# Kernel optimization log

Hardware: AMD Instinct MI355X
Metric: run time of the kernel (lower is better)

The kernel has to match this reference:

```python
import jax, jax.numpy as jnp
import numpy as np

B, M, H2, OUT = 32, 256, 32, 8  # H2 = 2*hidden_features

def setup_inputs() -> dict:
    key = jax.random.key(0)
    k1, k2, k3, k4, k5, k6 = jax.random.split(key, 6)
    x = jax.random.normal(k1, (B, M, 3), dtype=jnp.float32)
    mask = jax.random.randint(k2, (B, M, 1), 0, 2, dtype=jnp.int32)
    W1 = jax.random.normal(k3, (H2, 3), dtype=jnp.float32) * 0.1
    b1 = jax.random.normal(k4, (H2,), dtype=jnp.float32) * 0.1
    W2 = jax.random.normal(k5, (OUT, H2), dtype=jnp.float32) * 0.1
    b2 = jax.random.normal(k6, (OUT,), dtype=jnp.float32) * 0.1
    return {"x": x, "mask": mask, "W1": W1, "b1": b1, "W2": W2, "b2": b2}

def _safe_log(v):
    return jnp.log(jnp.where(v > 0, v, 1.0))

def reference(x, mask, W1, b1, W2, b2):
    # x: [B,M,3] = (eta, phi, log_pt); mask: [B,M,1]
    m = mask.astype(jnp.float32)
    me = (m @ jnp.swapaxes(m, -1, -2))[..., None]          # [B,M,M,1]

    eta, phi, ept = x[..., 0], x[..., 1], jnp.exp(x[..., 2])
    d_eta = eta[:, :, None] - eta[:, None, :]               # [B,M,M]
    d_phi = phi[:, :, None] - phi[:, None, :]
    dr2 = d_eta * d_eta + d_phi * d_phi

    # log dR (get_dr, is_log=True)
    dr_log = (0.5 * _safe_log(dr2))[..., None] * me
    # log kT (get_kt, is_log=True): min(pt_i, pt_j) * dR(linear, masked)
    dr_lin = jnp.sqrt(dr2)[..., None] * me
    kt = jnp.minimum(ept[:, :, None], ept[:, None, :])[..., None] * dr_lin
    kt_log = _safe_log(kt) * me
    # log m^2 (get_mass, is_log=True)
    m2 = 2.0 * ept[:, :, None] * ept[:, None, :] * (jnp.cosh(d_eta) - jnp.cos(d_phi))
    mass_log = _safe_log(m2)[..., None] * me

    feat = jnp.concatenate([mass_log, dr_log, kt_log], axis=-1)  # [B,M,M,3]

    h = jax.nn.leaky_relu(feat @ W1.T + b1, negative_slope=0.01)  # [B,M,M,H2]
    o = (h @ W2.T + b2) * me                                      # [B,M,M,OUT]
    # rearrange 'b n1 n2 h -> (b h) n1 n2'
    return jnp.transpose(o, (0, 3, 1, 2)).reshape(B * OUT, M, M)
```

## Files before the change

kernel.cpp:

```cpp
#include <hip/hip_runtime.h>
#include <math.h>

#define BB 32
#define MM 256
#define H2 32
#define NOUT 8

__device__ __forceinline__ float sinh_mag(float t) {
    float a  = fabsf(t);
    float e  = __expf(a);
    float big = 0.5f * (e - __builtin_amdgcn_rcpf(e));
    float t2 = t * t;
    float small = t + t * t2 * (1.0f/6.0f + t2 * (1.0f/120.0f));
    return (a < 0.5f) ? small : big;
}

__device__ __forceinline__ float sin_mag(float t) {
    float a  = fabsf(t);
    float t2 = t * t;
    float small = t + t * t2 * (-1.0f/6.0f + t2 * (1.0f/120.0f));
    float big = __sinf(t);
    return (a < 0.5f) ? small : big;
}

__global__ __launch_bounds__(256) void interaction_kernel(
    const float* __restrict__ x, const int* __restrict__ mask,
    const float* __restrict__ W1, const float* __restrict__ b1,
    const float* __restrict__ W2, const float* __restrict__ b2,
    float* __restrict__ out)
{
    const int bid = blockIdx.x;
    const int nb  = (bid & 7) * 1024 + (bid >> 3);
    const int b   = nb >> 8;
    const int i   = nb & 255;
    const int j   = threadIdx.x;

    float* op = out + ((size_t)(b * NOUT)) * (MM * MM) + (size_t)i * MM + j;
    const int PSTRIDE = MM * MM;

    const int mi = mask[b * MM + i];
    if (mi == 0) {
        #pragma unroll
        for (int p = 0; p < NOUT; ++p)
            __builtin_nontemporal_store(0.f, op + p * PSTRIDE);
        return;
    }

    const float eta_i = x[(b * MM + i) * 3 + 0];
    const float phi_i = x[(b * MM + i) * 3 + 1];
    const float lpt_i = x[(b * MM + i) * 3 + 2];

    const float eta_j = x[(b * MM + j) * 3 + 0];
    const float phi_j = x[(b * MM + j) * 3 + 1];
    const float lpt_j = x[(b * MM + j) * 3 + 2];
    const float mf    = mask[b * MM + j] ? 1.f : 0.f;

    const float dx  = eta_i - eta_j;
    const float dy  = phi_i - phi_j;
    const float dr2 = dx * dx + dy * dy;

    const float L      = (dr2 > 0.f) ? 0.5f * __logf(dr2) : 0.f;
    const float fdr    = L;
    const float fkt    = (dr2 > 0.f) ? fminf(lpt_i, lpt_j) + L : 0.f;

    const float sh = sinh_mag(0.5f * dx);
    const float sn = sin_mag(0.5f * dy);
    const float c  = 2.0f * (sh * sh + sn * sn);
    const float fmass = (c > 0.f) ? __logf(2.0f * c) + lpt_i + lpt_j : 0.f;

    float o[NOUT];
    #pragma unroll
    for (int p = 0; p < NOUT; ++p) o[p] = b2[p];

    #pragma unroll
    for (int k = 0; k < H2; ++k) {
        float z = b1[k];
        z = fmaf(fmass, W1[k * 3 + 0], z);
        z = fmaf(fdr,   W1[k * 3 + 1], z);
        z = fmaf(fkt,   W1[k * 3 + 2], z);
        z = (z >= 0.f) ? z : 0.01f * z;
        #pragma unroll
        for (int p = 0; p < NOUT; ++p)
            o[p] = fmaf(z, W2[p * H2 + k], o[p]);
    }

    #pragma unroll
    for (int p = 0; p < NOUT; ++p)
        __builtin_nontemporal_store(o[p] * mf, op + p * PSTRIDE);
}

extern "C" void kernel_launch(void* const* d_in, const int* in_sizes, int n_in,
                              void* d_out, int out_size, void* d_ws, size_t ws_size,
                              hipStream_t stream) {
    const float* x    = (const float*)d_in[0];
    const int*   mask = (const int*)d_in[1];
    const float* W1   = (const float*)d_in[2];
    const float* b1   = (const float*)d_in[3];
    const float* W2   = (const float*)d_in[4];
    const float* b2   = (const float*)d_in[5];
    float* out = (float*)d_out;

    dim3 grid(BB * MM);
    dim3 block(MM);
    interaction_kernel<<<grid, block, 0, stream>>>(x, mask, W1, b1, W2, b2, out);
}
```

Measured before the change: 24.53 us.

## Process four rows per block and stage outputs in LDS for float4 stores

Each block now handles four i-rows with 1024 threads. Results go into a shared-memory tile and are written back as float4 vectors covering 4 contiguous rows per output plane. This aims to cut the number of blocks and widen the global stores. In exchange it adds a __syncthreads and 32KB of LDS per block, and drops the nontemporal store hint and the early exit for masked rows.

New measurement: 55.37 us. +125.7%, slower.

```diff
diff --git a/kernel.cpp b/kernel.cpp
--- a/kernel.cpp
+++ b/kernel.cpp
@@ -23,70 +23,82 @@
     return (a < 0.5f) ? small : big;
 }
 
-__global__ __launch_bounds__(256) void interaction_kernel(
+__global__ __launch_bounds__(1024, 8) void interaction_kernel(
     const float* __restrict__ x, const int* __restrict__ mask,
     const float* __restrict__ W1, const float* __restrict__ b1,
     const float* __restrict__ W2, const float* __restrict__ b2,
     float* __restrict__ out)
 {
+    __shared__ float tile[NOUT * 4 * MM];
+
     const int bid = blockIdx.x;
-    const int nb  = (bid & 7) * 1024 + (bid >> 3);
-    const int b   = nb >> 8;
-    const int i   = nb & 255;
-    const int j   = threadIdx.x;
+    const int nb  = (bid & 7) * 256 + (bid >> 3);
+    const int b   = nb >> 6;
+    const int i0  = (nb & 63) << 2;
+    const int t   = threadIdx.x;
+    const int il  = t >> 8;
+    const int j   = t & 255;
 
-    float* op = out + ((size_t)(b * NOUT)) * (MM * MM) + (size_t)i * MM + j;
-    const int PSTRIDE = MM * MM;
-
+    const int i  = i0 + il;
     const int mi = mask[b * MM + i];
-    if (mi == 0) {
-        #pragma unroll
-        for (int p = 0; p < NOUT; ++p)
-            __builtin_nontemporal_store(0.f, op + p * PSTRIDE);
-        return;
-    }
-
-    const float eta_i = x[(b * MM + i) * 3 + 0];
-    const float phi_i = x[(b * MM + i) * 3 + 1];
-    const float lpt_i = x[(b * MM + i) * 3 + 2];
-
-    const float eta_j = x[(b * MM + j) * 3 + 0];
-    const float phi_j = x[(b * MM + j) * 3 + 1];
-    const float lpt_j = x[(b * MM + j) * 3 + 2];
-    const float mf    = mask[b * MM + j] ? 1.f : 0.f;
-
-    const float dx  = eta_i - eta_j;
-    const float dy  = phi_i - phi_j;
-    const float dr2 = dx * dx + dy * dy;
-
-    const float L      = (dr2 > 0.f) ? 0.5f * __logf(dr2) : 0.f;
-    const float fdr    = L;
-    const float fkt    = (dr2 > 0.f) ? fminf(lpt_i, lpt_j) + L : 0.f;
-
-    const float sh = sinh_mag(0.5f * dx);
-    const float sn = sin_mag(0.5f * dy);
-    const float c  = 2.0f * (sh * sh + sn * sn);
-    const float fmass = (c > 0.f) ? __logf(2.0f * c) + lpt_i + lpt_j : 0.f;
 
     float o[NOUT];
-    #pragma unroll
-    for (int p = 0; p < NOUT; ++p) o[p] = b2[p];
+    if (mi) {
+        const float eta_i = x[(b * MM + i) * 3 + 0];
+        const float phi_i = x[(b * MM + i) * 3 + 1];
+        const float lpt_i = x[(b * MM + i) * 3 + 2];
+        const float eta_j = x[(b * MM + j) * 3 + 0];
+        const float phi_j = x[(b * MM + j) * 3 + 1];
+        const float lpt_j = x[(b * MM + j) * 3 + 2];
+        const float mf    = mask[b * MM + j] ? 1.f : 0.f;
 
-    #pragma unroll
-    for (int k = 0; k < H2; ++k) {
-        float z = b1[k];
-        z = fmaf(fmass, W1[k * 3 + 0], z);
-        z = fmaf(fdr,   W1[k * 3 + 1], z);
-        z = fmaf(fkt,   W1[k * 3 + 2], z);
-        z = (z >= 0.f) ? z : 0.01f * z;
+        const float dx  = eta_i - eta_j;
+        const float dy  = phi_i - phi_j;
+        const float dr2 = dx * dx + dy * dy;
+
+        const float L   = (dr2 > 0.f) ? 0.5f * __logf(dr2) : 0.f;
+        const float fdr = L;
+        const float fkt = (dr2 > 0.f) ? fminf(lpt_i, lpt_j) + L : 0.f;
+
+        const float sh = sinh_mag(0.5f * dx);
+        const float sn = sin_mag(0.5f * dy);
+        const float c  = 2.0f * (sh * sh + sn * sn);
+        const float fmass = (c > 0.f) ? __logf(2.0f * c) + lpt_i + lpt_j : 0.f;
+
         #pragma unroll
-        for (int p = 0; p < NOUT; ++p)
-            o[p] = fmaf(z, W2[p * H2 + k], o[p]);
+        for (int p = 0; p < NOUT; ++p) o[p] = b2[p];
+
+        #pragma unroll
+        for (int k = 0; k < H2; ++k) {
+            float z = b1[k];
+            z = fmaf(fmass, W1[k * 3 + 0], z);
+            z = fmaf(fdr,   W1[k * 3 + 1], z);
+            z = fmaf(fkt,   W1[k * 3 + 2], z);
+            z = (z >= 0.f) ? z : 0.01f * z;
+            #pragma unroll
+            for (int p = 0; p < NOUT; ++p)
+                o[p] = fmaf(z, W2[p * H2 + k], o[p]);
+        }
+        #pragma unroll
+        for (int p = 0; p < NOUT; ++p) o[p] *= mf;
+    } else {
+        #pragma unroll
+        for (int p = 0; p < NOUT; ++p) o[p] = 0.f;
     }
 
     #pragma unroll
-    for (int p = 0; p < NOUT; ++p)
-        __builtin_nontemporal_store(o[p] * mf, op + p * PSTRIDE);
+    for (int p = 0; p < NOUT; ++p) tile[p * 1024 + t] = o[p];
+    __syncthreads();
+
+    const float4* tile4 = (const float4*)tile;
+    float4* out4 = (float4*)out;
+    #pragma unroll
+    for (int q = t; q < 2048; q += 1024) {
+        const int p   = q >> 8;
+        const int idx = q & 255;
+        out4[(size_t)(b * NOUT + p) * (MM * MM / 4) + i0 * (MM / 4) + idx] =
+            tile4[q];
+    }
 }
 
 extern "C" void kernel_launch(void* const* d_in, const int* in_sizes, int n_in,
@@ -100,7 +112,7 @@
     const float* b2   = (const float*)d_in[5];
     float* out = (float*)d_out;
 
-    dim3 grid(BB * MM);
-    dim3 block(MM);
+    dim3 grid(BB * MM / 4);
+    dim3 block(1024);
     interaction_kernel<<<grid, block, 0, stream>>>(x, mask, W1, b1, W2, b2, out);
 }
```

## Compact active j-columns per row via ballot so masked lanes skip MLP work

Applied to the files above, without the earlier changes.

Each block now runs a wave ballot and prefix count over the j mask, building a shared permutation that packs unmasked columns first. Threads with t<K compute features and the MLP for column perm[t], and the remaining threads write zeros, so whole waves of masked columns skip the arithmetic instead of computing and multiplying by zero. The cost is two __syncthreads, some shared-memory traffic, and scattered stores (op+j with permuted j) that break fully coalesced writes within a wave.

Result: slower. 32.87 us (+34.0%).

```diff
diff --git a/kernel.cpp b/kernel.cpp
--- a/kernel.cpp
+++ b/kernel.cpp
@@ -29,64 +29,89 @@
     const float* __restrict__ W2, const float* __restrict__ b2,
     float* __restrict__ out)
 {
+    __shared__ int perm[MM];
+    __shared__ int wcnt[4];
+
     const int bid = blockIdx.x;
     const int nb  = (bid & 7) * 1024 + (bid >> 3);
     const int b   = nb >> 8;
     const int i   = nb & 255;
-    const int j   = threadIdx.x;
+    const int t   = threadIdx.x;
+    const int w   = t >> 6;
+    const int l   = t & 63;
 
-    float* op = out + ((size_t)(b * NOUT)) * (MM * MM) + (size_t)i * MM + j;
+    float* op = out + ((size_t)(b * NOUT)) * (MM * MM) + (size_t)i * MM;
     const int PSTRIDE = MM * MM;
 
     const int mi = mask[b * MM + i];
     if (mi == 0) {
         #pragma unroll
         for (int p = 0; p < NOUT; ++p)
-            __builtin_nontemporal_store(0.f, op + p * PSTRIDE);
+            __builtin_nontemporal_store(0.f, op + p * PSTRIDE + t);
         return;
     }
 
-    const float eta_i = x[(b * MM + i) * 3 + 0];
-    const float phi_i = x[(b * MM + i) * 3 + 1];
-    const float lpt_i = x[(b * MM + i) * 3 + 2];
+    const int mj = mask[b * MM + t];
+    const unsigned long long bm = __ballot(mj != 0);
+    if (l == 0) wcnt[w] = __popcll(bm);
+    __syncthreads();
+    const int c0 = wcnt[0], c1 = wcnt[1], c2 = wcnt[2], c3 = wcnt[3];
+    const int K  = c0 + c1 + c2 + c3;
+    int abase = 0, ibase = K;
+    if (w > 0) { abase += c0; ibase += 64 - c0; }
+    if (w > 1) { abase += c1; ibase += 64 - c1; }
+    if (w > 2) { abase += c2; ibase += 64 - c2; }
+    const int lt = __popcll(bm & ((1ull << l) - 1ull));
+    if (mj) perm[abase + lt] = t;
+    else    perm[ibase + (l - lt)] = t;
+    __syncthreads();
 
-    const float eta_j = x[(b * MM + j) * 3 + 0];
-    const float phi_j = x[(b * MM + j) * 3 + 1];
-    const float lpt_j = x[(b * MM + j) * 3 + 2];
-    const float mf    = mask[b * MM + j] ? 1.f : 0.f;
-
-    const float dx  = eta_i - eta_j;
-    const float dy  = phi_i - phi_j;
-    const float dr2 = dx * dx + dy * dy;
-
-    const float L      = (dr2 > 0.f) ? 0.5f * __logf(dr2) : 0.f;
-    const float fdr    = L;
-    const float fkt    = (dr2 > 0.f) ? fminf(lpt_i, lpt_j) + L : 0.f;
-
-    const float sh = sinh_mag(0.5f * dx);
-    const float sn = sin_mag(0.5f * dy);
-    const float c  = 2.0f * (sh * sh + sn * sn);
-    const float fmass = (c > 0.f) ? __logf(2.0f * c) + lpt_i + lpt_j : 0.f;
+    const int j = perm[t];
 
     float o[NOUT];
-    #pragma unroll
-    for (int p = 0; p < NOUT; ++p) o[p] = b2[p];
+    if (t < K) {
+        const float eta_i = x[(b * MM + i) * 3 + 0];
+        const float phi_i = x[(b * MM + i) * 3 + 1];
+        const float lpt_i = x[(b * MM + i) * 3 + 2];
+        const float eta_j = x[(b * MM + j) * 3 + 0];
+        const float phi_j = x[(b * MM + j) * 3 + 1];
+        const float lpt_j = x[(b * MM + j) * 3 + 2];
 
-    #pragma unroll
-    for (int k = 0; k < H2; ++k) {
-        float z = b1[k];
-        z = fmaf(fmass, W1[k * 3 + 0], z);
-        z = fmaf(fdr,   W1[k * 3 + 1], z);
-        z = fmaf(fkt,   W1[k * 3 + 2], z);
-        z = (z >= 0.f) ? z : 0.01f * z;
+        const float dx  = eta_i - eta_j;
+        const float dy  = phi_i - phi_j;
+        const float dr2 = dx * dx + dy * dy;
+
+        const float L   = (dr2 > 0.f) ? 0.5f * __logf(dr2) : 0.f;
+        const float fdr = L;
+        const float fkt = (dr2 > 0.f) ? fminf(lpt_i, lpt_j) + L : 0.f;
+
+        const float sh = sinh_mag(0.5f * dx);
+        const float sn = sin_mag(0.5f * dy);
+        const float c  = 2.0f * (sh * sh + sn * sn);
+        const float fmass = (c > 0.f) ? __logf(2.0f * c) + lpt_i + lpt_j : 0.f;
+
         #pragma unroll
-        for (int p = 0; p < NOUT; ++p)
-            o[p] = fmaf(z, W2[p * H2 + k], o[p]);
+        for (int p = 0; p < NOUT; ++p) o[p] = b2[p];
+
+        #pragma unroll
+        for (int k = 0; k < H2; ++k) {
+            float z = b1[k];
+            z = fmaf(fmass, W1[k * 3 + 0], z);
+            z = fmaf(fdr,   W1[k * 3 + 1], z);
+            z = fmaf(fkt,   W1[k * 3 + 2], z);
+            z = (z >= 0.f) ? z : 0.01f * z;
+            #pragma unroll
+            for (int p = 0; p < NOUT; ++p)
+                o[p] = fmaf(z, W2[p * H2 + k], o[p]);
+        }
+    } else {
+        #pragma unroll
+        for (int p = 0; p < NOUT; ++p) o[p] = 0.f;
     }
 
     #pragma unroll
     for (int p = 0; p < NOUT; ++p)
-        __builtin_nontemporal_store(o[p] * mf, op + p * PSTRIDE);
+        __builtin_nontemporal_store(o[p], op + p * PSTRIDE + j);
 }
 
 extern "C" void kernel_launch(void* const* d_in, const int* in_sizes, int n_in,
```
